# Performance work log

Hardware: AMD Instinct MI355X
Metric: run time of the kernel (lower is better)

## Reference

```python
import jax, jax.numpy as jnp
from jax import lax
import numpy as np

LATENT = 512
LABEL = 128
BATCH = 1024


def _maxpool2(x):
    # 2x2 max pool, stride 2, NCHW
    return lax.reduce_window(x, -jnp.inf, lax.max, (1, 1, 2, 2), (1, 1, 2, 2), 'VALID')


def _encoder(x, c1w, c1b, c2w, c2b, fw, fb):
    dn = ('NCHW', 'OIHW', 'NCHW')
    y = lax.conv_general_dilated(x, c1w, (1, 1), 'SAME', dimension_numbers=dn)
    y = _maxpool2(jax.nn.relu(y + c1b[None, :, None, None]))  # [B,32,14,14]
    y = lax.conv_general_dilated(y, c2w, (1, 1), 'SAME', dimension_numbers=dn)
    y = _maxpool2(jax.nn.relu(y + c2b[None, :, None, None]))  # [B,64,7,7]
    y = y.reshape(y.shape[0], -1)                              # [B,3136]
    return y @ fw.T + fb                                       # [B,latent]


def _hopfield_w(rep):
    # rho = mean over ALL elements (matches torch.mean(x))
    rho = jnp.mean(rep)
    t = rep - rho                      # [label, latent]
    w = t.T @ t                        # sum of rank-1 outer products
    w = w * (1.0 - jnp.eye(w.shape[0], dtype=w.dtype))  # zero diagonal
    return w / LABEL


def _clustering(lat, w):
    # batched fixed-length Hopfield relaxation with min-energy tracking
    s0 = jnp.tanh(lat)                 # [B,L]
    B = s0.shape[0]

    def step(carry, _):
        s, min_e, min_s = carry
        prev = lax.stop_gradient(s)    # torch detaches prev_s each iter
        s_new = jnp.abs(prev) * jnp.sign(prev @ w.T)      # [B,L]
        e = -jnp.einsum('bi,ij,bj->b', s_new, w, s_new)    # [B]
        better = e < min_e
        min_e = jnp.where(better, e, min_e)
        min_s = jnp.where(better[:, None], s_new, min_s)
        return (s_new, min_e, min_s), None

    init = (s0, jnp.full((B,), jnp.inf, dtype=s0.dtype), jnp.zeros_like(s0))
    (_, _, min_s), _ = lax.scan(step, init, None, length=LATENT)
    return min_s


def setup_inputs() -> dict:
    key = jax.random.key(0)
    ks = jax.random.split(key, 11)
    d = {}
    d['image'] = jax.random.normal(ks[0], (BATCH, 1, 28, 28), dtype=jnp.float32)
    d['label_images'] = jax.random.uniform(ks[1], (LABEL, 1, 28, 28), dtype=jnp.float32)
    d['conv1_w'] = jax.random.normal(ks[2], (32, 1, 5, 5), dtype=jnp.float32) * 0.1
    d['conv1_b'] = jnp.zeros((32,), dtype=jnp.float32)
    d['conv2_w'] = jax.random.normal(ks[3], (64, 32, 5, 5), dtype=jnp.float32) * 0.05
    d['conv2_b'] = jnp.zeros((64,), dtype=jnp.float32)
    d['fc1_w'] = jax.random.normal(ks[4], (LATENT, 64 * 7 * 7), dtype=jnp.float32) * 0.02
    d['fc1_b'] = jnp.zeros((LATENT,), dtype=jnp.float32)
    d['fcn_w'] = jax.random.normal(ks[5], (LABEL, LATENT), dtype=jnp.float32) * 0.05
    d['fcn_b'] = jnp.zeros((LABEL,), dtype=jnp.float32)
    return d


def reference(image, label_images, conv1_w, conv1_b, conv2_w, conv2_b,
              fc1_w, fc1_b, fcn_w, fcn_b):
    rep = jnp.tanh(_encoder(label_images, conv1_w, conv1_b, conv2_w, conv2_b, fc1_w, fc1_b))  # [label,L]
    lat = _encoder(image, conv1_w, conv1_b, conv2_w, conv2_b, fc1_w, fc1_b)                    # [B,L]
    # FCN on detached latents (torch: .clone().detach())
    label = jax.nn.softmax(lax.stop_gradient(lat) @ fcn_w.T + fcn_b, axis=1)                   # [B,label]
    w = _hopfield_w(rep)                                                                        # [L,L]
    min_s = _clustering(lat, w)                                                                 # [B,L]
    out = jax.nn.softmax(jnp.abs(min_s @ rep.T), axis=1)                                        # [B,label]
    return (out, label)
```

## Files before the change

kernel.cpp:

```cpp
#include <hip/hip_runtime.h>
#include <hip/hip_bf16.h>
#include <math.h>

#define BATCH 1024
#define LABEL 128
#define LATENT 512
#define NTOT 1152

typedef short short8 __attribute__((ext_vector_type(8)));
typedef float f32x16 __attribute__((ext_vector_type(16)));

__device__ __forceinline__ unsigned short f2bf(float f) {
    __hip_bfloat16 h = __float2bfloat16(f);
    return *(unsigned short*)&h;
}
__device__ __forceinline__ float bf2f(unsigned short u) {
    __hip_bfloat16 h; *(unsigned short*)&h = u;
    return __bfloat162float(h);
}

#define BSTR ((size_t)512 * 3136)
#define ASTR ((size_t)NTOT * 3136)
#define A2STR ((size_t)BATCH * 512)
#define W2STR ((size_t)LABEL * 512)


__global__ __launch_bounds__(256) void conv1_pool(const float* __restrict__ image,
                                                  const float* __restrict__ limg,
                                                  const float* __restrict__ wt,
                                                  const float* __restrict__ bias,
                                                  unsigned short* __restrict__ o1b) {
    const int n = blockIdx.x;
    const float* in = (n < BATCH) ? (image + (size_t)n * 784)
                                  : (limg + (size_t)(n - BATCH) * 784);
    __shared__ float pin[32][32];
    __shared__ float wts[32 * 25];
    const int tid = threadIdx.x;
    unsigned short* ob = o1b + (size_t)n * 12800;
    for (int i = tid; i < 256; i += 256) {
        int pl_ = i >> 7, r = i & 127;
        ob[pl_ * 6400 + 6272 + r] = 0;
    }
    for (int idx = tid; idx < 32 * 32; idx += 256) ((float*)pin)[idx] = 0.f;
    __syncthreads();
    for (int idx = tid; idx < 784; idx += 256) {
        int y = idx / 28, x = idx % 28;
        pin[y + 2][x + 2] = in[idx];
    }
    for (int idx = tid; idx < 800; idx += 256) wts[idx] = wt[idx];
    __syncthreads();
    const int oc = tid & 31;
    float wk[25];
    #pragma unroll
    for (int k = 0; k < 25; ++k) wk[k] = wts[oc * 25 + k];
    const float b = bias[oc];
    const int slot_lo = (oc & 7);
    const int gq = oc >> 3;
    for (int it = 0; it < 2; ++it) {
        const int py = (tid >> 5) + it * 8;
        if (py >= 14) continue;
        #pragma unroll
        for (int xh = 0; xh < 2; ++xh) {
            const int acol = xh ? 12 : 0;
            const int off = xh ? 2 : 0;
            float a0[14], a1[14];
            #pragma unroll
            for (int c = 0; c < 14; ++c) { a0[c] = b; a1[c] = b; }
            #pragma unroll
            for (int t = 0; t < 6; ++t) {
                float row[20];
                const float4* rp = (const float4*)&pin[2 * py + t][acol];
                #pragma unroll
                for (int v = 0; v < 5; ++v) {
                    float4 f = rp[v];
                    row[4 * v] = f.x; row[4 * v + 1] = f.y;
                    row[4 * v + 2] = f.z; row[4 * v + 3] = f.w;
                }
                if (t < 5) {
                    #pragma unroll
                    for (int kx = 0; kx < 5; ++kx) {
                        float w0 = wk[t * 5 + kx];
                        #pragma unroll
                        for (int c = 0; c < 14; ++c)
                            a0[c] = fmaf(row[c + kx + off], w0, a0[c]);
                    }
                }
                if (t >= 1) {
                    #pragma unroll
                    for (int kx = 0; kx < 5; ++kx) {
                        float w1 = wk[(t - 1) * 5 + kx];
                        #pragma unroll
                        for (int c = 0; c < 14; ++c)
                            a1[c] = fmaf(row[c + kx + off], w1, a1[c]);
                    }
                }
            }
            #pragma unroll
            for (int px = 0; px < 7; ++px) {
                float v = fmaxf(fmaxf(a0[2 * px], a0[2 * px + 1]),
                                fmaxf(a1[2 * px], a1[2 * px + 1]));
                v = fmaxf(v, 0.f);
                unsigned short b1 = f2bf(v);
                unsigned short b2 = f2bf(v - bf2f(b1));
                int p = py * 14 + 7 * xh + px;
                int offo = p * 32 + (((gq ^ (p >> 1)) & 3) << 3) + slot_lo;
                ob[offo] = b1; ob[6400 + offo] = b2;
            }
        }
    }
}

__global__ __launch_bounds__(256) void prep(const float* __restrict__ c2w,
                                            const float* __restrict__ f1w,
                                            const float* __restrict__ fnw,
                                            unsigned short* __restrict__ Bf,
                                            unsigned short* __restrict__ Bw2,
                                            unsigned short* __restrict__ Bn2) {
    int idx = blockIdx.x * 256 + threadIdx.x;
    if (idx < 102400) {
        int j = idx & 7, lane = (idx >> 3) & 63, ocT = (idx >> 9) & 1, s = idx >> 10;
        int q = lane >> 5, nn = lane & 31;
        int k = 16 * s + 8 * q + j;
        int tap = k >> 5, ic = k & 31;
        int oc = 32 * ocT + nn;
        float v = c2w[oc * 800 + ic * 25 + tap];
        unsigned short b1 = f2bf(v);
        unsigned short b2 = f2bf(v - bf2f(b1));
        size_t base = ((size_t)(s * 2 + ocT) * 2) * 512 + lane * 8 + j;
        Bf[base] = b1; Bf[base + 512] = b2;
        return;
    }
    int i2 = idx - 102400;
    if (i2 < 512 * 3136) {
        float v = f1w[i2];
        unsigned short b1 = f2bf(v);
        unsigned short b2 = f2bf(v - bf2f(b1));
        Bw2[i2] = b1; Bw2[BSTR + i2] = b2;
        return;
    }
    int i3 = i2 - 512 * 3136;
    if (i3 >= 128 * 512) return;
    float v = fnw[i3];
    unsigned short b1 = f2bf(v);
    unsigned short b2 = f2bf(v - bf2f(b1));
    Bn2[i3] = b1; Bn2[W2STR + i3] = b2;
}

__global__ __launch_bounds__(256) void conv2_mfma(const unsigned short* __restrict__ o1b,
                                                  const unsigned short* __restrict__ Bf,
                                                  const float* __restrict__ bias,
                                                  unsigned short* __restrict__ out2) {
    const int n = blockIdx.x;
    __shared__ __align__(16) unsigned short pl[12800];
    const int tid = threadIdx.x;
    const int lane = tid & 63, wv = tid >> 6;
    const int ocT = wv & 1, mh = wv >> 1;

    {
        const float4* src = (const float4*)(o1b + (size_t)n * 12800);
        float4* dst = (float4*)pl;
        for (int i = tid; i < 1600; i += 256) dst[i] = src[i];
    }
    __syncthreads();

    const int m_ = lane & 31, q = lane >> 5;
    int ym[4], xm[4], mm[4], tvv[4];
    #pragma unroll
    for (int tt = 0; tt < 4; ++tt) {
        int t = 4 * mh + tt;
        tvv[tt] = (t < 7);
        int m = 32 * t + m_;
        mm[tt] = m;
        ym[tt] = m / 14;
        xm[tt] = m - 14 * ym[tt];
    }
    f32x16 acc[4];
    {
        float bs = bias[32 * ocT + m_];
        #pragma unroll
        for (int tt = 0; tt < 4; ++tt)
        #pragma unroll
        for (int r = 0; r < 16; ++r) acc[tt][r] = bs;
    }

    for (int s = 0; s < 50; ++s) {
        const unsigned short* bp = Bf + ((size_t)(s * 2 + ocT) * 2) * 512 + lane * 8;
        short8 b1 = *(const short8*)(bp);
        short8 b2 = *(const short8*)(bp + 512);
        int kb = 16 * s + 8 * q;
        int tap = kb >> 5, ic0 = kb & 31, g = ic0 >> 3;
        int ky = (tap * 13) >> 6;
        int kx = tap - ky * 5;
        int iyk = ky - 2, ixk = kx - 2;
        int pq2 = iyk * 14 + ixk;
        short8 a1[4], a2[4];
        #pragma unroll
        for (int tt = 0; tt < 4; ++tt) {
            int iy = ym[tt] + iyk, ix = xm[tt] + ixk;
            int valid = tvv[tt] & ((unsigned)iy < 14u) & ((unsigned)ix < 14u);
            int cpt = valid ? (mm[tt] + pq2) : 196;
            int addr = cpt * 32 + (((g ^ (cpt >> 1)) & 3) << 3);
            a1[tt] = *(const short8*)(pl + addr);
            a2[tt] = *(const short8*)(pl + 6400 + addr);
        }
        #pragma unroll
        for (int tt = 0; tt < 4; ++tt)
            acc[tt] = __builtin_amdgcn_mfma_f32_32x32x16_bf16(a1[tt], b1, acc[tt], 0, 0, 0);
        #pragma unroll
        for (int tt = 0; tt < 4; ++tt)
            acc[tt] = __builtin_amdgcn_mfma_f32_32x32x16_bf16(a1[tt], b2, acc[tt], 0, 0, 0);
        #pragma unroll
        for (int tt = 0; tt < 4; ++tt)
            acc[tt] = __builtin_amdgcn_mfma_f32_32x32x16_bf16(a2[tt], b1, acc[tt], 0, 0, 0);
    }
    __syncthreads();

    float* hx = (float*)pl;
    {
        const int oc = 32 * ocT + m_;
        #pragma unroll
        for (int tt = 0; tt < 4; ++tt)
        #pragma unroll
        for (int e = 0; e < 8; ++e) {
            const int reg = 2 * e;
            const int r = (reg & 3) + 8 * (reg >> 2) + 4 * q;
            const int m = 32 * (4 * mh + tt) + r;
            if (m < 196) {
                float xm2 = fmaxf(acc[tt][reg], acc[tt][reg + 1]);
                int y = (m * 2341) >> 15;
                int px = (m - 14 * y) >> 1;
                hx[(y * 7 + px) * 65 + oc] = xm2;
            }
        }
    }
    __syncthreads();

    for (int idx = tid; idx < 3136; idx += 256) {
        int oc2 = (idx * 2675) >> 17;
        int p = idx - 49 * oc2;
        int py = (p * 9363) >> 16;
        int px = p - 7 * py;
        float v = fmaxf(hx[(2 * py * 7 + px) * 65 + oc2],
                        hx[((2 * py + 1) * 7 + px) * 65 + oc2]);
        v = fmaxf(v, 0.f);
        unsigned short b1 = f2bf(v);
        unsigned short b2 = f2bf(v - bf2f(b1));
        size_t o = (size_t)n * 3136 + idx;
        out2[o] = b1; out2[ASTR + o] = b2;
    }
}

__global__ __launch_bounds__(256) void fc1_mfma(const unsigned short* __restrict__ A2,
                                                const unsigned short* __restrict__ B2,
                                                float* __restrict__ part) {
    __shared__ unsigned short As[2][2048];
    __shared__ unsigned short Bs[2][2048];
    const int tid = threadIdx.x;
    const int n0 = blockIdx.x * 64, m0 = blockIdx.y * 64;
    const int koff = blockIdx.z * 448;
    const int lr = tid >> 2, g = tid & 3;
    const int slot = (((g ^ (lr >> 1)) & 3) << 3);
    const int lane = tid & 63, wv = tid >> 6;
    const int nq = wv & 1, mq = wv >> 1;
    const int q = lane >> 5, l31 = lane & 31;
    const int rA = 32 * nq + l31, rB = 32 * mq + l31;
    f32x16 acc;
    #pragma unroll
    for (int r = 0; r < 16; ++r) acc[r] = 0.f;

    for (int bk = 0; bk < 448; bk += 32) {
        const size_t ka = (size_t)(koff + bk + (g << 3));
        short8 av[2], bv[2];
        #pragma unroll
        for (int p = 0; p < 2; ++p) {
            av[p] = *(const short8*)(A2 + p * ASTR + (size_t)(n0 + lr) * 3136 + ka);
            bv[p] = *(const short8*)(B2 + p * BSTR + (size_t)(m0 + lr) * 3136 + ka);
        }
        __syncthreads();
        #pragma unroll
        for (int p = 0; p < 2; ++p) {
            *(short8*)&As[p][(lr << 5) + slot] = av[p];
            *(short8*)&Bs[p][(lr << 5) + slot] = bv[p];
        }
        __syncthreads();
        #pragma unroll
        for (int s2 = 0; s2 < 32; s2 += 16) {
            const int gg = (s2 + (q << 3)) >> 3;
            const int sa = (((gg ^ (rA >> 1)) & 3) << 3);
            const int sb = (((gg ^ (rB >> 1)) & 3) << 3);
            short8 a1 = *(const short8*)&As[0][(rA << 5) + sa];
            short8 a2 = *(const short8*)&As[1][(rA << 5) + sa];
            short8 b1 = *(const short8*)&Bs[0][(rB << 5) + sb];
            short8 b2 = *(const short8*)&Bs[1][(rB << 5) + sb];
            acc = __builtin_amdgcn_mfma_f32_32x32x16_bf16(a1, b1, acc, 0, 0, 0);
            acc = __builtin_amdgcn_mfma_f32_32x32x16_bf16(a1, b2, acc, 0, 0, 0);
            acc = __builtin_amdgcn_mfma_f32_32x32x16_bf16(a2, b1, acc, 0, 0, 0);
        }
    }
    float* pb = part + (size_t)blockIdx.z * NTOT * 512;
    #pragma unroll
    for (int reg = 0; reg < 16; ++reg) {
        int nn = n0 + 32 * nq + (reg & 3) + 8 * (reg >> 2) + 4 * q;
        int mmo = m0 + 32 * mq + l31;
        pb[(size_t)nn * 512 + mmo] = acc[reg];
    }
}

__global__ __launch_bounds__(256) void fc1_reduce(const float* __restrict__ part,
                                                  const float* __restrict__ bias,
                                                  float* __restrict__ lat,
                                                  unsigned short* __restrict__ lat2,
                                                  float* __restrict__ rep) {
    int idx = blockIdx.x * 256 + threadIdx.x;
    int m = idx & 511;
    float v = bias[m];
    #pragma unroll
    for (int kz = 0; kz < 7; ++kz) v += part[(size_t)kz * NTOT * 512 + idx];
    if (idx < BATCH * 512) {
        lat[idx] = v;
        unsigned short b1 = f2bf(v);
        lat2[idx] = b1;
        lat2[A2STR + idx] = f2bf(v - bf2f(b1));
    } else {
        rep[idx - BATCH * 512] = tanhf(v);
    }
}

__global__ __launch_bounds__(256) void fcn_mfma(const unsigned short* __restrict__ A2,
                                                const unsigned short* __restrict__ B2,
                                                float* __restrict__ logits) {
    __shared__ unsigned short As[2][2048];
    __shared__ unsigned short Bs[2][2048];
    const int tid = threadIdx.x;
    const int n0 = blockIdx.x * 64, m0 = blockIdx.y * 64;
    const int lr = tid >> 2, g = tid & 3;
    const int slot = (((g ^ (lr >> 1)) & 3) << 3);
    const int lane = tid & 63, wv = tid >> 6;
    const int nq = wv & 1, mq = wv >> 1;
    const int q = lane >> 5, l31 = lane & 31;
    const int rA = 32 * nq + l31, rB = 32 * mq + l31;
    f32x16 acc;
    #pragma unroll
    for (int r = 0; r < 16; ++r) acc[r] = 0.f;

    for (int bk = 0; bk < 512; bk += 32) {
        const size_t ka = (size_t)(bk + (g << 3));
        short8 av[2], bv[2];
        #pragma unroll
        for (int p = 0; p < 2; ++p) {
            av[p] = *(const short8*)(A2 + p * A2STR + (size_t)(n0 + lr) * 512 + ka);
            bv[p] = *(const short8*)(B2 + p * W2STR + (size_t)(m0 + lr) * 512 + ka);
        }
        __syncthreads();
        #pragma unroll
        for (int p = 0; p < 2; ++p) {
            *(short8*)&As[p][(lr << 5) + slot] = av[p];
            *(short8*)&Bs[p][(lr << 5) + slot] = bv[p];
        }
        __syncthreads();
        #pragma unroll
        for (int s2 = 0; s2 < 32; s2 += 16) {
            const int gg = (s2 + (q << 3)) >> 3;
            const int sa = (((gg ^ (rA >> 1)) & 3) << 3);
            const int sb = (((gg ^ (rB >> 1)) & 3) << 3);
            short8 a1 = *(const short8*)&As[0][(rA << 5) + sa];
            short8 a2 = *(const short8*)&As[1][(rA << 5) + sa];
            short8 b1 = *(const short8*)&Bs[0][(rB << 5) + sb];
            short8 b2 = *(const short8*)&Bs[1][(rB << 5) + sb];
            acc = __builtin_amdgcn_mfma_f32_32x32x16_bf16(a1, b1, acc, 0, 0, 0);
            acc = __builtin_amdgcn_mfma_f32_32x32x16_bf16(a1, b2, acc, 0, 0, 0);
            acc = __builtin_amdgcn_mfma_f32_32x32x16_bf16(a2, b1, acc, 0, 0, 0);
        }
    }
    #pragma unroll
    for (int reg = 0; reg < 16; ++reg) {
        int nn = n0 + 32 * nq + (reg & 3) + 8 * (reg >> 2) + 4 * q;
        int mmo = m0 + 32 * mq + l31;
        logits[(size_t)nn * 128 + mmo] = acc[reg];
    }
}

__global__ __launch_bounds__(128) void fcn_softmax2(const float* __restrict__ logits,
                                                    const float* __restrict__ fb,
                                                    float* __restrict__ out) {
    const int b = blockIdx.x;
    const int j = threadIdx.x;
    __shared__ float red[128];
    float acc = logits[(size_t)b * 128 + j] + fb[j];
    red[j] = acc;
    __syncthreads();
    for (int off = 64; off >= 1; off >>= 1) {
        if (j < off) red[j] = fmaxf(red[j], red[j + off]);
        __syncthreads();
    }
    float mx = red[0];
    __syncthreads();
    float ex = expf(acc - mx);
    red[j] = ex;
    __syncthreads();
    for (int off = 64; off >= 1; off >>= 1) {
        if (j < off) red[j] += red[j + off];
        __syncthreads();
    }
    out[(size_t)b * 128 + j] = ex / red[0];
}

__global__ __launch_bounds__(256) void rho_kernel(const float* __restrict__ rep,
                                                  float* __restrict__ rho) {
    __shared__ float red[256];
    const int tid = threadIdx.x;
    float s = 0.f;
    for (int i = tid; i < LABEL * LATENT; i += 256) s += rep[i];
    red[tid] = s;
    __syncthreads();
    for (int off = 128; off >= 1; off >>= 1) {
        if (tid < off) red[tid] += red[tid + off];
        __syncthreads();
    }
    if (tid == 0) rho[0] = red[0] / (float)(LABEL * LATENT);
}

__global__ __launch_bounds__(256) void t_kernel(const float* __restrict__ rep,
                                                const float* __restrict__ rho,
                                                float* __restrict__ tT) {
    __shared__ float tile[64][65];
    const int tid = threadIdx.x;
    const int i0 = blockIdx.x * 64, k0 = blockIdx.y * 64;
    const int tx = tid & 63, ty4 = tid >> 6;
    const float r0 = rho[0];
    #pragma unroll
    for (int rr = 0; rr < 16; ++rr) {
        int kk = ty4 * 16 + rr;
        tile[kk][tx] = rep[(size_t)(k0 + kk) * 512 + i0 + tx];
    }
    __syncthreads();
    #pragma unroll
    for (int rr = 0; rr < 16; ++rr) {
        int ii = ty4 * 16 + rr;
        tT[(size_t)(i0 + ii) * 128 + k0 + tx] = tile[tx][ii] - r0;
    }
}

__global__ __launch_bounds__(256) void w_kernel(const float* __restrict__ tT,
                                                float* __restrict__ w) {
    int idx = blockIdx.x * 256 + threadIdx.x;
    int i = idx >> 9, j = idx & 511;
    const float4* a = (const float4*)(tT + i * 128);
    const float4* b = (const float4*)(tT + j * 128);
    float acc = 0.f;
    #pragma unroll 8
    for (int q = 0; q < 32; ++q) {
        float4 av = a[q], bv = b[q];
        acc += av.x * bv.x + av.y * bv.y + av.z * bv.z + av.w * bv.w;
    }
    w[idx] = (i == j) ? 0.f : acc * (1.f / 128.f);
}

__global__ __launch_bounds__(256) void hinit(const float* __restrict__ lat,
                                             const float* __restrict__ w,
                                             float* __restrict__ hmat) {
    __shared__ float As[16][68];
    __shared__ float Bs[16][68];
    const int tid = threadIdx.x;
    const int n0 = blockIdx.x * 64, m0 = blockIdx.y * 64;
    const int lr = tid >> 2;
    const int lk = (tid & 3) * 4;
    const int ty = tid >> 4, tx = tid & 15;
    float c[4][4] = {};
    for (int k0 = 0; k0 < 512; k0 += 16) {
        float4 a4 = *(const float4*)(lat + (size_t)(n0 + lr) * 512 + k0 + lk);
        float4 b4 = *(const float4*)(w + (size_t)(m0 + lr) * 512 + k0 + lk);
        a4.x = tanhf(a4.x); a4.y = tanhf(a4.y); a4.z = tanhf(a4.z); a4.w = tanhf(a4.w);
        __syncthreads();
        As[lk + 0][lr] = a4.x; As[lk + 1][lr] = a4.y; As[lk + 2][lr] = a4.z; As[lk + 3][lr] = a4.w;
        Bs[lk + 0][lr] = b4.x; Bs[lk + 1][lr] = b4.y; Bs[lk + 2][lr] = b4.z; Bs[lk + 3][lr] = b4.w;
        __syncthreads();
        #pragma unroll
        for (int kk = 0; kk < 16; ++kk) {
            float av[4], bv[4];
            #pragma unroll
            for (int i = 0; i < 4; ++i) av[i] = As[kk][ty * 4 + i];
            #pragma unroll
            for (int j = 0; j < 4; ++j) bv[j] = Bs[kk][tx * 4 + j];
            #pragma unroll
            for (int i = 0; i < 4; ++i)
            #pragma unroll
            for (int j = 0; j < 4; ++j) c[i][j] += av[i] * bv[j];
        }
    }
    #pragma unroll
    for (int i = 0; i < 4; ++i)
    #pragma unroll
    for (int j = 0; j < 4; ++j)
        hmat[(size_t)(n0 + ty * 4 + i) * 512 + m0 + tx * 4 + j] = c[i][j];
}

__device__ __forceinline__ float sgnf(float x) {
    return (x > 0.f) ? 1.f : ((x < 0.f) ? -1.f : 0.f);
}

__global__ __launch_bounds__(256) void clustering(const float* __restrict__ lat,
                                                  const float* __restrict__ hmat,
                                                  const float* __restrict__ w,
                                                  const float* __restrict__ rep,
                                                  float* __restrict__ out) {
    const int tid = threadIdx.x;
    const int row = blockIdx.x;
    __shared__ float mins[512];
    __shared__ float red[256];
    __shared__ float part_e[4];
    __shared__ int part_c[4];
    __shared__ float min_e_s;
    __shared__ int copyf_s;
    __shared__ int donef_s;
    __shared__ int cnt_s;
    __shared__ int jidx[512];
    __shared__ float jdel[512];
    const int i0 = 2 * tid, i1 = 2 * tid + 1;
    const int wave = tid >> 6, lane = tid & 63;

    float sm10, sm11, sm20, sm21, h0, h1;
    {
        sm10 = tanhf(lat[(size_t)row * 512 + i0]);
        sm11 = tanhf(lat[(size_t)row * 512 + i1]);
        sm20 = sm10; sm21 = sm11;
        h0 = hmat[(size_t)row * 512 + i0];
        h1 = hmat[(size_t)row * 512 + i1];
    }
    if (tid == 0) { min_e_s = INFINITY; donef_s = 0; cnt_s = 0; }
    __syncthreads();

    for (int k = 1; k <= 512; ++k) {
        float sn0 = fabsf(sm10) * sgnf(h0);
        float sn1 = fabsf(sm11) * sgnf(h1);
        int cy = (sn0 == sm20 && sn1 == sm21) ? 1 : 0;
        if (sn0 != sm10) {
            int p = atomicAdd(&cnt_s, 1);
            jidx[p] = i0; jdel[p] = sn0 - sm10;
        }
        if (sn1 != sm11) {
            int p = atomicAdd(&cnt_s, 1);
            jidx[p] = i1; jdel[p] = sn1 - sm11;
        }
        #pragma unroll
        for (int m = 32; m >= 1; m >>= 1) cy &= __shfl_xor(cy, m, 64);
        if (lane == 0) part_c[wave] = cy;
        __syncthreads();

        {
            const int c = cnt_s;
            #pragma unroll 8
            for (int t = 0; t < c; ++t) {
                const int j = jidx[t];
                const float d = jdel[t];
                const float2 wvv = *(const float2*)(w + (size_t)j * 512 + i0);
                h0 = fmaf(d, wvv.x, h0);
                h1 = fmaf(d, wvv.y, h1);
            }
        }
        float ep = sn0 * h0 + sn1 * h1;
        #pragma unroll
        for (int m = 32; m >= 1; m >>= 1) ep += __shfl_xor(ep, m, 64);
        if (lane == 0) part_e[wave] = ep;
        __syncthreads();

        if (tid == 0) {
            float e = -(part_e[0] + part_e[1] + part_e[2] + part_e[3]);
            int better = e < min_e_s;
            if (better) min_e_s = e;
            copyf_s = better;
            int fl = part_c[0] & part_c[1] & part_c[2] & part_c[3];
            int fixedp = (cnt_s == 0);
            int cyc = (k >= 2) && fl;
            if (fixedp || cyc) donef_s = 1;
            cnt_s = 0;
        }
        __syncthreads();

        if (copyf_s) { mins[i0] = sn0; mins[i1] = sn1; }
        sm20 = sm10; sm21 = sm11;
        sm10 = sn0;  sm11 = sn1;
        if (donef_s) break;
    }
    __syncthreads();

    const int j = tid & 127, half = tid >> 7;
    {
        const float4* rr = (const float4*)(rep + (size_t)j * 512 + half * 256);
        const float4* ms = (const float4*)(&mins[half * 256]);
        float p = 0.f;
        #pragma unroll 8
        for (int q = 0; q < 64; ++q) {
            float4 rv = rr[q], mv = ms[q];
            p += rv.x * mv.x + rv.y * mv.y + rv.z * mv.z + rv.w * mv.w;
        }
        red[tid] = p;
        __syncthreads();
        float v = 0.f;
        if (tid < 128) { v = fabsf(red[tid] + red[tid + 128]); red[tid] = v; }
        __syncthreads();
        for (int off = 64; off >= 1; off >>= 1) {
            if (tid < off) red[tid] = fmaxf(red[tid], red[tid + off]);
            __syncthreads();
        }
        float mx = red[0];
        __syncthreads();
        float ex = 0.f;
        if (tid < 128) { ex = expf(v - mx); red[tid] = ex; }
        __syncthreads();
        for (int off = 64; off >= 1; off >>= 1) {
            if (tid < off) red[tid] += red[tid + off];
            __syncthreads();
        }
        if (tid < 128) out[(size_t)row * 128 + tid] = ex / red[0];
    }
}

extern "C" void kernel_launch(void* const* d_in, const int* in_sizes, int n_in,
                              void* d_out, int out_size, void* d_ws, size_t ws_size,
                              hipStream_t stream) {
    const float* image = (const float*)d_in[0];
    const float* limg  = (const float*)d_in[1];
    const float* c1w   = (const float*)d_in[2];
    const float* c1b   = (const float*)d_in[3];
    const float* c2w   = (const float*)d_in[4];
    const float* c2b   = (const float*)d_in[5];
    const float* f1w   = (const float*)d_in[6];
    const float* f1b   = (const float*)d_in[7];
    const float* fnw   = (const float*)d_in[8];
    const float* fnb   = (const float*)d_in[9];
    float* out = (float*)d_out;
    float* ws  = (float*)d_ws;

    unsigned short* o1b  = (unsigned short*)ws;
    unsigned short* out2 = o1b + (size_t)NTOT * 12800;
    float* lat  = (float*)(out2 + 2 * ASTR);
    float* rep  = lat + (size_t)BATCH * 512;
    float* tT   = rep + (size_t)LABEL * 512;
    float* wmat = tT + (size_t)512 * 128;
    float* rho  = wmat + (size_t)512 * 512;
    unsigned short* Bw2   = (unsigned short*)(rho + 16);
    unsigned short* Bfrag = Bw2 + 2 * BSTR;
    float* hmat = (float*)(Bfrag + 102400);
    unsigned short* lat2 = (unsigned short*)(hmat + A2STR);
    unsigned short* fnw2 = lat2 + 2 * A2STR;
    float* logits = (float*)(fnw2 + 2 * W2STR);
    float* part = (float*)ws;

    const int prep_total = 102400 + 512 * 3136 + 128 * 512;
    hipLaunchKernelGGL(prep, dim3((prep_total + 255) / 256), dim3(256), 0, stream,
                       c2w, f1w, fnw, Bfrag, Bw2, fnw2);
    hipLaunchKernelGGL(conv1_pool, dim3(NTOT), dim3(256), 0, stream, image, limg, c1w, c1b, o1b);
    hipLaunchKernelGGL(conv2_mfma, dim3(NTOT), dim3(256), 0, stream, o1b, Bfrag, c2b, out2);
    hipLaunchKernelGGL(fc1_mfma, dim3(NTOT / 64, 512 / 64, 7), dim3(256), 0, stream,
                       out2, Bw2, part);
    hipLaunchKernelGGL(fc1_reduce, dim3(NTOT * 512 / 256), dim3(256), 0, stream,
                       part, f1b, lat, lat2, rep);
    hipLaunchKernelGGL(fcn_mfma, dim3(16, 2), dim3(256), 0, stream, lat2, fnw2, logits);
    hipLaunchKernelGGL(fcn_softmax2, dim3(BATCH), dim3(128), 0, stream, logits, fnb,
                       out + (size_t)BATCH * LABEL);
    hipLaunchKernelGGL(rho_kernel, dim3(1), dim3(256), 0, stream, rep, rho);
    hipLaunchKernelGGL(t_kernel, dim3(8, 2), dim3(256), 0, stream, rep, rho, tT);
    hipLaunchKernelGGL(w_kernel, dim3(1024), dim3(256), 0, stream, tT, wmat);
    hipLaunchKernelGGL(hinit, dim3(BATCH / 64, 512 / 64), dim3(256), 0, stream, lat, wmat, hmat);
    hipLaunchKernelGGL(clustering, dim3(BATCH), dim3(256), 0, stream,
                       lat, hmat, wmat, rep, out);
}
```

Baseline: 398.8 us.

## Fuse FCN GEMM with softmax and precompute first two Hopfield steps as batched GEMMs

The FCN logits GEMM and its softmax become one kernel where each block computes a full 64x128 logits tile and applies bias plus softmax in shared memory. This removes the logits round-trip and a launch. The first Hopfield iteration (s1 and its field h1) now comes from two tiled GEMM kernels, so the per-row clustering loop starts at step 2 with the initial energy precomputed. The trade-off is an extra GEMM launch, and the fused FCN runs on only 16 blocks, so it has low parallelism.

```diff
diff --git a/kernel.cpp b/kernel.cpp
--- a/kernel.cpp
+++ b/kernel.cpp
@@ -326,83 +326,89 @@
     }
 }
 
-__global__ __launch_bounds__(256) void fcn_mfma(const unsigned short* __restrict__ A2,
-                                                const unsigned short* __restrict__ B2,
-                                                float* __restrict__ logits) {
+__global__ __launch_bounds__(256) void fcn_fused(const unsigned short* __restrict__ A2,
+                                                 const unsigned short* __restrict__ B2,
+                                                 const float* __restrict__ fb,
+                                                 float* __restrict__ out) {
     __shared__ unsigned short As[2][2048];
-    __shared__ unsigned short Bs[2][2048];
-    const int tid = threadIdx.x;
-    const int n0 = blockIdx.x * 64, m0 = blockIdx.y * 64;
+    __shared__ unsigned short Bs[2][4096];
+    __shared__ float Ls[64][132];
+    __shared__ float fbs[128], rmax[64], rsum[64];
+    const int tid = threadIdx.x;
+    const int n0 = blockIdx.x * 64;
     const int lr = tid >> 2, g = tid & 3;
-    const int slot = (((g ^ (lr >> 1)) & 3) << 3);
+    const int slotA = (((g ^ (lr >> 1)) & 3) << 3);
+    const int lrB2 = lr + 64;
+    const int slotB2 = (((g ^ (lrB2 >> 1)) & 3) << 3);
     const int lane = tid & 63, wv = tid >> 6;
     const int nq = wv & 1, mq = wv >> 1;
     const int q = lane >> 5, l31 = lane & 31;
-    const int rA = 32 * nq + l31, rB = 32 * mq + l31;
-    f32x16 acc;
-    #pragma unroll
-    for (int r = 0; r < 16; ++r) acc[r] = 0.f;
+    const int rA = 32 * nq + l31;
+    if (tid < 128) fbs[tid] = fb[tid];
+    f32x16 acc[2];
+    #pragma unroll
+    for (int j = 0; j < 2; ++j)
+    #pragma unroll
+    for (int r = 0; r < 16; ++r) acc[j][r] = 0.f;
 
     for (int bk = 0; bk < 512; bk += 32) {
         const size_t ka = (size_t)(bk + (g << 3));
-        short8 av[2], bv[2];
+        short8 av[2], blo[2], bhi[2];
         #pragma unroll
         for (int p = 0; p < 2; ++p) {
-            av[p] = *(const short8*)(A2 + p * A2STR + (size_t)(n0 + lr) * 512 + ka);
-            bv[p] = *(const short8*)(B2 + p * W2STR + (size_t)(m0 + lr) * 512 + ka);
+            av[p]  = *(const short8*)(A2 + p * A2STR + (size_t)(n0 + lr) * 512 + ka);
+            blo[p] = *(const short8*)(B2 + p * W2STR + (size_t)lr * 512 + ka);
+            bhi[p] = *(const short8*)(B2 + p * W2STR + (size_t)lrB2 * 512 + ka);
         }
         __syncthreads();
         #pragma unroll
         for (int p = 0; p < 2; ++p) {
-            *(short8*)&As[p][(lr << 5) + slot] = av[p];
-            *(short8*)&Bs[p][(lr << 5) + slot] = bv[p];
+            *(short8*)&As[p][(lr << 5) + slotA] = av[p];
+            *(short8*)&Bs[p][(lr << 5) + slotA] = blo[p];
+            *(short8*)&Bs[p][(lrB2 << 5) + slotB2] = bhi[p];
         }
         __syncthreads();
         #pragma unroll
         for (int s2 = 0; s2 < 32; s2 += 16) {
             const int gg = (s2 + (q << 3)) >> 3;
             const int sa = (((gg ^ (rA >> 1)) & 3) << 3);
-            const int sb = (((gg ^ (rB >> 1)) & 3) << 3);
             short8 a1 = *(const short8*)&As[0][(rA << 5) + sa];
             short8 a2 = *(const short8*)&As[1][(rA << 5) + sa];
-            short8 b1 = *(const short8*)&Bs[0][(rB << 5) + sb];
-            short8 b2 = *(const short8*)&Bs[1][(rB << 5) + sb];
-            acc = __builtin_amdgcn_mfma_f32_32x32x16_bf16(a1, b1, acc, 0, 0, 0);
-            acc = __builtin_amdgcn_mfma_f32_32x32x16_bf16(a1, b2, acc, 0, 0, 0);
-            acc = __builtin_amdgcn_mfma_f32_32x32x16_bf16(a2, b1, acc, 0, 0, 0);
-        }
-    }
+            #pragma unroll
+            for (int j = 0; j < 2; ++j) {
+                const int rB = 64 * mq + 32 * j + l31;
+                const int sb = (((gg ^ (rB >> 1)) & 3) << 3);
+                short8 b1 = *(const short8*)&Bs[0][(rB << 5) + sb];
+                short8 b2 = *(const short8*)&Bs[1][(rB << 5) + sb];
+                acc[j] = __builtin_amdgcn_mfma_f32_32x32x16_bf16(a1, b1, acc[j], 0, 0, 0);
+                acc[j] = __builtin_amdgcn_mfma_f32_32x32x16_bf16(a1, b2, acc[j], 0, 0, 0);
+                acc[j] = __builtin_amdgcn_mfma_f32_32x32x16_bf16(a2, b1, acc[j], 0, 0, 0);
+            }
+        }
+    }
+    __syncthreads();
+    #pragma unroll
+    for (int j = 0; j < 2; ++j)
     #pragma unroll
     for (int reg = 0; reg < 16; ++reg) {
-        int nn = n0 + 32 * nq + (reg & 3) + 8 * (reg >> 2) + 4 * q;
-        int mmo = m0 + 32 * mq + l31;
-        logits[(size_t)nn * 128 + mmo] = acc[reg];
-    }
-}
-
-__global__ __launch_bounds__(128) void fcn_softmax2(const float* __restrict__ logits,
-                                                    const float* __restrict__ fb,
-                                                    float* __restrict__ out) {
-    const int b = blockIdx.x;
-    const int j = threadIdx.x;
-    __shared__ float red[128];
-    float acc = logits[(size_t)b * 128 + j] + fb[j];
-    red[j] = acc;
-    __syncthreads();
-    for (int off = 64; off >= 1; off >>= 1) {
-        if (j < off) red[j] = fmaxf(red[j], red[j + off]);
-        __syncthreads();
-    }
-    float mx = red[0];
-    __syncthreads();
-    float ex = expf(acc - mx);
-    red[j] = ex;
-    __syncthreads();
-    for (int off = 64; off >= 1; off >>= 1) {
-        if (j < off) red[j] += red[j + off];
-        __syncthreads();
-    }
-    out[(size_t)b * 128 + j] = ex / red[0];
+        int nnl = 32 * nq + (reg & 3) + 8 * (reg >> 2) + 4 * q;
+        int mml = 64 * mq + 32 * j + l31;
+        Ls[nnl][mml] = acc[j][reg];
+    }
+    __syncthreads();
+    if (tid < 64) {
+        float mx = -1e30f;
+        for (int c = 0; c < 128; ++c) mx = fmaxf(mx, Ls[tid][c] + fbs[c]);
+        float sm = 0.f;
+        for (int c = 0; c < 128; ++c) sm += expf(Ls[tid][c] + fbs[c] - mx);
+        rmax[tid] = mx; rsum[tid] = sm;
+    }
+    __syncthreads();
+    for (int i = tid; i < 8192; i += 256) {
+        int r = i >> 7, c = i & 127;
+        out[(size_t)(n0 + r) * 128 + c] =
+            expf(Ls[r][c] + fbs[c] - rmax[r]) / rsum[r];
+    }
 }
 
 __global__ __launch_bounds__(256) void rho_kernel(const float* __restrict__ rep,
@@ -456,9 +462,13 @@
     w[idx] = (i == j) ? 0.f : acc * (1.f / 128.f);
 }
 
-__global__ __launch_bounds__(256) void hinit(const float* __restrict__ lat,
-                                             const float* __restrict__ w,
-                                             float* __restrict__ hmat) {
+__device__ __forceinline__ float sgnf(float x) {
+    return (x > 0.f) ? 1.f : ((x < 0.f) ? -1.f : 0.f);
+}
+
+__global__ __launch_bounds__(256) void s1init(const float* __restrict__ lat,
+                                              const float* __restrict__ w,
+                                              float* __restrict__ s1buf) {
     __shared__ float As[16][68];
     __shared__ float Bs[16][68];
     const int tid = threadIdx.x;
@@ -489,18 +499,57 @@
         }
     }
     #pragma unroll
+    for (int i = 0; i < 4; ++i) {
+        const int nn = n0 + ty * 4 + i;
+        float4 lv = *(const float4*)(lat + (size_t)nn * 512 + m0 + tx * 4);
+        float s0a[4] = {tanhf(lv.x), tanhf(lv.y), tanhf(lv.z), tanhf(lv.w)};
+        #pragma unroll
+        for (int j = 0; j < 4; ++j)
+            s1buf[(size_t)nn * 512 + m0 + tx * 4 + j] = fabsf(s0a[j]) * sgnf(c[i][j]);
+    }
+}
+
+__global__ __launch_bounds__(256) void h1init(const float* __restrict__ s1buf,
+                                              const float* __restrict__ w,
+                                              float* __restrict__ hmat2) {
+    __shared__ float As[16][68];
+    __shared__ float Bs[16][68];
+    const int tid = threadIdx.x;
+    const int n0 = blockIdx.x * 64, m0 = blockIdx.y * 64;
+    const int lr = tid >> 2;
+    const int lk = (tid & 3) * 4;
+    const int ty = tid >> 4, tx = tid & 15;
+    float c[4][4] = {};
+    for (int k0 = 0; k0 < 512; k0 += 16) {
+        float4 a4 = *(const float4*)(s1buf + (size_t)(n0 + lr) * 512 + k0 + lk);
+        float4 b4 = *(const float4*)(w + (size_t)(m0 + lr) * 512 + k0 + lk);
+        __syncthreads();
+        As[lk + 0][lr] = a4.x; As[lk + 1][lr] = a4.y; As[lk + 2][lr] = a4.z; As[lk + 3][lr] = a4.w;
+        Bs[lk + 0][lr] = b4.x; Bs[lk + 1][lr] = b4.y; Bs[lk + 2][lr] = b4.z; Bs[lk + 3][lr] = b4.w;
+        __syncthreads();
+        #pragma unroll
+        for (int kk = 0; kk < 16; ++kk) {
+            float av[4], bv[4];
+            #pragma unroll
+            for (int i = 0; i < 4; ++i) av[i] = As[kk][ty * 4 + i];
+            #pragma unroll
+            for (int j = 0; j < 4; ++j) bv[j] = Bs[kk][tx * 4 + j];
+            #pragma unroll
+            for (int i = 0; i < 4; ++i)
+            #pragma unroll
+            for (int j = 0; j < 4; ++j) c[i][j] += av[i] * bv[j];
+        }
+    }
+    #pragma unroll
     for (int i = 0; i < 4; ++i)
     #pragma unroll
     for (int j = 0; j < 4; ++j)
-        hmat[(size_t)(n0 + ty * 4 + i) * 512 + m0 + tx * 4 + j] = c[i][j];
-}
-
-__device__ __forceinline__ float sgnf(float x) {
-    return (x > 0.f) ? 1.f : ((x < 0.f) ? -1.f : 0.f);
+        hmat2[(size_t)(n0 + ty * 4 + i) * 512 + m0 + tx * 4 + j] = c[i][j];
 }
 
 __global__ __launch_bounds__(256) void clustering(const float* __restrict__ lat,
-                                                  const float* __restrict__ hmat,
+                                                  const float* __restrict__ s1buf,
+                                                  const float* __restrict__ hmat2,
                                                   const float* __restrict__ w,
                                                   const float* __restrict__ rep,
                                                   float* __restrict__ out) {
@@ -519,18 +568,25 @@
     const int i0 = 2 * tid, i1 = 2 * tid + 1;
     const int wave = tid >> 6, lane = tid & 63;
 
-    float sm10, sm11, sm20, sm21, h0, h1;
+    float sm20 = tanhf(lat[(size_t)row * 512 + i0]);
+    float sm21 = tanhf(lat[(size_t)row * 512 + i1]);
+    float sm10 = s1buf[(size_t)row * 512 + i0];
+    float sm11 = s1buf[(size_t)row * 512 + i1];
+    float h0 = hmat2[(size_t)row * 512 + i0];
+    float h1 = hmat2[(size_t)row * 512 + i1];
+    mins[i0] = sm10; mins[i1] = sm11;
     {
-        sm10 = tanhf(lat[(size_t)row * 512 + i0]);
-        sm11 = tanhf(lat[(size_t)row * 512 + i1]);
-        sm20 = sm10; sm21 = sm11;
-        h0 = hmat[(size_t)row * 512 + i0];
-        h1 = hmat[(size_t)row * 512 + i1];
-    }
-    if (tid == 0) { min_e_s = INFINITY; donef_s = 0; cnt_s = 0; }
-    __syncthreads();
-
-    for (int k = 1; k <= 512; ++k) {
+        float ep = sm10 * h0 + sm11 * h1;
+        #pragma unroll
+        for (int m = 32; m >= 1; m >>= 1) ep += __shfl_xor(ep, m, 64);
+        if (lane == 0) part_e[wave] = ep;
+    }
+    if (tid == 0) { donef_s = 0; cnt_s = 0; }
+    __syncthreads();
+    if (tid == 0) min_e_s = -(part_e[0] + part_e[1] + part_e[2] + part_e[3]);
+    __syncthreads();
+
+    for (int k = 2; k <= 512; ++k) {
         float sn0 = fabsf(sm10) * sgnf(h0);
         float sn1 = fabsf(sm11) * sgnf(h1);
         int cy = (sn0 == sm20 && sn1 == sm21) ? 1 : 0;
@@ -571,8 +627,7 @@
             copyf_s = better;
             int fl = part_c[0] & part_c[1] & part_c[2] & part_c[3];
             int fixedp = (cnt_s == 0);
-            int cyc = (k >= 2) && fl;
-            if (fixedp || cyc) donef_s = 1;
+            if (fixedp || fl) donef_s = 1;
             cnt_s = 0;
         }
         __syncthreads();
@@ -641,10 +696,10 @@
     float* rho  = wmat + (size_t)512 * 512;
     unsigned short* Bw2   = (unsigned short*)(rho + 16);
     unsigned short* Bfrag = Bw2 + 2 * BSTR;
-    float* hmat = (float*)(Bfrag + 102400);
-    unsigned short* lat2 = (unsigned short*)(hmat + A2STR);
+    float* s1buf = (float*)(Bfrag + 102400);
+    unsigned short* lat2 = (unsigned short*)(s1buf + A2STR);
     unsigned short* fnw2 = lat2 + 2 * A2STR;
-    float* logits = (float*)(fnw2 + 2 * W2STR);
+    float* hmat2 = (float*)(fnw2 + 2 * W2STR);
     float* part = (float*)ws;
 
     const int prep_total = 102400 + 512 * 3136 + 128 * 512;
@@ -656,13 +711,15 @@
                        out2, Bw2, part);
     hipLaunchKernelGGL(fc1_reduce, dim3(NTOT * 512 / 256), dim3(256), 0, stream,
                        part, f1b, lat, lat2, rep);
-    hipLaunchKernelGGL(fcn_mfma, dim3(16, 2), dim3(256), 0, stream, lat2, fnw2, logits);
-    hipLaunchKernelGGL(fcn_softmax2, dim3(BATCH), dim3(128), 0, stream, logits, fnb,
-                       out + (size_t)BATCH * LABEL);
+    hipLaunchKernelGGL(fcn_fused, dim3(BATCH / 64), dim3(256), 0, stream,
+                       lat2, fnw2, fnb, out + (size_t)BATCH * LABEL);
     hipLaunchKernelGGL(rho_kernel, dim3(1), dim3(256), 0, stream, rep, rho);
     hipLaunchKernelGGL(t_kernel, dim3(8, 2), dim3(256), 0, stream, rep, rho, tT);
     hipLaunchKernelGGL(w_kernel, dim3(1024), dim3(256), 0, stream, tT, wmat);
-    hipLaunchKernelGGL(hinit, dim3(BATCH / 64, 512 / 64), dim3(256), 0, stream, lat, wmat, hmat);
+    hipLaunchKernelGGL(s1init, dim3(BATCH / 64, 512 / 64), dim3(256), 0, stream,
+                       lat, wmat, s1buf);
+    hipLaunchKernelGGL(h1init, dim3(BATCH / 64, 512 / 64), dim3(256), 0, stream,
+                       s1buf, wmat, hmat2);
     hipLaunchKernelGGL(clustering, dim3(BATCH), dim3(256), 0, stream,
-                       lat, hmat, wmat, rep, out);
-}
+                       lat, s1buf, hmat2, wmat, rep, out);
+}
```

After: 428.7 us. +7.5%, slower.
